# Performance work log

Hardware: AMD Instinct MI355X
Metric: run time of the kernel (lower is better)

Reference implementation:

```python
import jax, jax.numpy as jnp
import numpy as np

B, Q, C = 8, 100, 1024
H, W = 64, 64
NH = 16
HD = C // NH
SCALE = HD ** -0.5
LN_EPS = 1e-5


def setup_inputs() -> dict:
    key = jax.random.key(0)
    ks = jax.random.split(key, 8)
    xav = lambda k, shp: jax.random.normal(k, shp, jnp.float32) * (2.0 / (shp[0] + shp[-1])) ** 0.5
    return {
        "tgt": jax.random.normal(ks[0], (B, Q, C), jnp.float32),
        "memory": jax.random.normal(ks[1], (B, H, W, C), jnp.float32),
        "memory_pos_emb": jax.random.normal(ks[2], (B, H, W, C), jnp.float32),
        "query_pos_emb": jax.random.normal(ks[3], (B, Q, C), jnp.float32),
        "Wq": xav(ks[4], (C, C)),
        "Wk": xav(ks[5], (C, C)),
        "Wv": xav(ks[6], (C, C)),
        "Wo": xav(ks[7], (C, C)),
        "bo": jnp.zeros((C,), jnp.float32),
        "ln_gamma": jnp.ones((C,), jnp.float32),
        "ln_beta": jnp.zeros((C,), jnp.float32),
    }


def _layernorm(x, g, b):
    mu = jnp.mean(x, axis=-1, keepdims=True)
    var = jnp.var(x, axis=-1, keepdims=True)
    return (x - mu) * jax.lax.rsqrt(var + LN_EPS) * g + b


def reference(tgt, memory, memory_pos_emb, query_pos_emb, Wq, Wk, Wv, Wo, bo, ln_gamma, ln_beta):
    # flatten spatial dims: [B,H,W,C] -> [B,K,C]
    mem = memory.reshape(B, H * W, C)
    mpos = memory_pos_emb.reshape(B, H * W, C)
    q_in = tgt + query_pos_emb          # [B,Q,C]
    k_in = mem + mpos                    # [B,K,C]
    # projections (torch Linear: x @ W.T), split heads -> [B,nh,*,hd]
    q = (q_in @ Wq.T).reshape(B, Q, NH, HD).transpose(0, 2, 1, 3)
    k = (k_in @ Wk.T).reshape(B, -1, NH, HD).transpose(0, 2, 1, 3)
    v = (mem @ Wv.T).reshape(B, -1, NH, HD).transpose(0, 2, 1, 3)
    dots = jnp.einsum('bhid,bhjd->bhij', q, k) * SCALE   # [B,nh,Q,K]
    # slot attention: softmax over QUERY axis, then renormalize over keys
    attn = jax.nn.softmax(dots, axis=2)
    attn = attn / (jnp.sum(attn, axis=-1, keepdims=True) + 1e-8)
    updates = jnp.einsum('bhij,bhjd->bhid', attn, v)     # [B,nh,Q,hd]
    updates = updates.transpose(0, 2, 1, 3).reshape(B, Q, C)
    out = updates @ Wo.T + bo
    # residual (dropout is identity in eval) + post-LayerNorm
    return _layernorm(tgt + out, ln_gamma, ln_beta)
```

## Files before the change

kernel.cpp:

```cpp
#include <hip/hip_runtime.h>

typedef unsigned short u16;
typedef __attribute__((ext_vector_type(8))) short bf16x8;
typedef __attribute__((ext_vector_type(4))) short bf16x4;
typedef __attribute__((ext_vector_type(4))) float f32x4;
typedef __attribute__((ext_vector_type(4))) unsigned short u16x4;
typedef __attribute__((ext_vector_type(8))) unsigned short u16x8;
typedef __attribute__((ext_vector_type(4))) int i32x4;
typedef __attribute__((ext_vector_type(4))) float f4;

#define DI __device__ __forceinline__


DI u16 f2bf(float f){
  unsigned int u = __float_as_uint(f);
  return (u16)((u + 0x7FFFu + ((u >> 16) & 1u)) >> 16);
}

DI void gl_lds16(const void* g, void* l){
  __builtin_amdgcn_global_load_lds((const __attribute__((address_space(1))) unsigned int*)g,
                                   (__attribute__((address_space(3))) unsigned int*)l, 16, 0, 0);
}

__global__ __launch_bounds__(256) void prep_kv(const float* __restrict__ mem,
                                               const float* __restrict__ mpos,
                                               u16* __restrict__ kA, u16* __restrict__ vA){
  const int t = blockIdx.x * 256 + threadIdx.x;
  #pragma unroll
  for (int i = 0; i < 4; ++i){
    const size_t g = (size_t)t + (size_t)i * 1048576;
    f4 m0 = __builtin_nontemporal_load((const f4*)mem  + g * 2);
    f4 m1 = __builtin_nontemporal_load((const f4*)mem  + g * 2 + 1);
    f4 p0 = __builtin_nontemporal_load((const f4*)mpos + g * 2);
    f4 p1 = __builtin_nontemporal_load((const f4*)mpos + g * 2 + 1);
    u16x8 k, v;
    #pragma unroll
    for (int j = 0; j < 4; ++j){
      k[j]     = f2bf(m0[j] + p0[j]);  v[j]     = f2bf(m0[j]);
      k[j + 4] = f2bf(m1[j] + p1[j]);  v[j + 4] = f2bf(m1[j]);
    }
    ((u16x8*)kA)[g] = k;
    ((u16x8*)vA)[g] = v;
  }
}

__global__ __launch_bounds__(256) void prep_qw(const float* __restrict__ tgt,
                                               const float* __restrict__ qpos,
                                               const float* __restrict__ Wq, const float* __restrict__ Wk,
                                               const float* __restrict__ Wv, const float* __restrict__ Wo,
                                               u16* __restrict__ qA, u16* __restrict__ Wbf){
  int gid = blockIdx.x * 256 + threadIdx.x;
  const int NQ4 = 819200 / 4;
  if (gid < NQ4){
    f4 a = ((const f4*)tgt)[gid];
    f4 b = ((const f4*)qpos)[gid];
    u16x4 r;
    #pragma unroll
    for (int j = 0; j < 4; ++j) r[j] = f2bf(a[j] + b[j]);
    ((u16x4*)qA)[gid] = r;
  } else {
    int wid = gid - NQ4;
    int sel = wid >> 18;
    int off = wid & 262143;
    const float* W = (sel == 0) ? Wq : (sel == 1) ? Wk : (sel == 2) ? Wv : Wo;
    f4 w = ((const f4*)W)[off];
    u16x4 r;
    #pragma unroll
    for (int j = 0; j < 4; ++j) r[j] = f2bf(w[j]);
    ((u16x4*)(Wbf))[(size_t)sel * 262144 + off] = r;
  }
}

DI void gemm256_body(const u16* __restrict__ A, const u16* __restrict__ Bw,
                     u16* __restrict__ Cb, float scale, int sbid, int tid, char* lds)
{
  const int l = tid & 63, w = tid >> 6;
  const int mb = sbid >> 2, nb = sbid & 3;
  const int m0 = mb * 256, n0 = nb * 256;
  const int fr = l & 15, fg = l >> 4;
  const int wm = w >> 2, wn = w & 3;

  char* ldsA  = lds + wm * 8192 + l * 16;
  char* ldsB  = lds + 32768 + wn * 4096 + l * 16;
  char* ldsS0 = lds + w * 1024;
  char* ldsS1 = lds + (8 + w) * 1024;
  const u16* gA0 = A  + (size_t)(m0 + w * 16 + fr) * 1024 + fg * 8;
  const u16* gA1 = A  + (size_t)(m0 + (8 + w) * 16 + fr) * 1024 + fg * 8;
  const u16* gB0 = Bw + (size_t)(n0 + w * 16 + fr) * 1024 + fg * 8;
  const u16* gB1 = Bw + (size_t)(n0 + (8 + w) * 16 + fr) * 1024 + fg * 8;

  auto stA = [&](int pp, int kh, int kt){
    const int o = kt * 64 + kh * 32;
    gl_lds16(gA0 + o, ldsS0 + pp * 65536 + kh * 16384);
    gl_lds16(gA1 + o, ldsS1 + pp * 65536 + kh * 16384);
  };
  auto stB = [&](int pp, int kh, int kt){
    const int o = kt * 64 + kh * 32;
    gl_lds16(gB0 + o, ldsS0 + pp * 65536 + 32768 + kh * 16384);
    gl_lds16(gB1 + o, ldsS1 + pp * 65536 + 32768 + kh * 16384);
  };
  auto rdA4 = [&](bf16x8* av, int pp, int kh, int mfb){
    #pragma unroll
    for (int i = 0; i < 4; ++i)
      av[i] = *(const bf16x8*)(ldsA + pp * 65536 + kh * 16384 + (mfb + i) * 1024);
  };
  auto rdB4 = [&](bf16x8* bv, int pp, int kh){
    #pragma unroll
    for (int i = 0; i < 4; ++i)
      bv[i] = *(const bf16x8*)(ldsB + pp * 65536 + kh * 16384 + i * 1024);
  };

  f32x4 acc[8][4] = {};

  stA(0, 0, 0); stB(0, 0, 0); stA(0, 1, 0); stB(0, 1, 0);
  stA(1, 0, 1); stB(1, 0, 1);
  asm volatile("s_waitcnt vmcnt(8)" ::: "memory");
  __builtin_amdgcn_s_barrier();

  auto ktbody = [&](int P, int kt){
    const int kt1 = (kt + 1 > 15) ? 15 : kt + 1;
    const int kt2 = (kt + 2 > 15) ? 15 : kt + 2;
    bf16x8 av[4], bv[4];

    rdA4(av, P, 0, 0); rdB4(bv, P, 0);
    stA(P ^ 1, 1, kt1);
    __builtin_amdgcn_s_barrier();
    __builtin_amdgcn_s_setprio(1);
    #pragma unroll
    for (int i = 0; i < 4; ++i)
      #pragma unroll
      for (int n = 0; n < 4; ++n)
        acc[i][n] = __builtin_amdgcn_mfma_f32_16x16x32_bf16(av[i], bv[n], acc[i][n], 0, 0, 0);
    __builtin_amdgcn_s_setprio(0);
    __builtin_amdgcn_s_barrier();

    rdA4(av, P, 0, 4);
    stB(P ^ 1, 1, kt1);
    asm volatile("s_waitcnt vmcnt(8)" ::: "memory");
    __builtin_amdgcn_s_barrier();
    __builtin_amdgcn_s_setprio(1);
    #pragma unroll
    for (int i = 0; i < 4; ++i)
      #pragma unroll
      for (int n = 0; n < 4; ++n)
        acc[4 + i][n] = __builtin_amdgcn_mfma_f32_16x16x32_bf16(av[i], bv[n], acc[4 + i][n], 0, 0, 0);
    __builtin_amdgcn_s_setprio(0);
    __builtin_amdgcn_s_barrier();

    rdA4(av, P, 1, 0); rdB4(bv, P, 1);
    stA(P, 0, kt2);
    __builtin_amdgcn_s_barrier();
    __builtin_amdgcn_s_setprio(1);
    #pragma unroll
    for (int i = 0; i < 4; ++i)
      #pragma unroll
      for (int n = 0; n < 4; ++n)
        acc[i][n] = __builtin_amdgcn_mfma_f32_16x16x32_bf16(av[i], bv[n], acc[i][n], 0, 0, 0);
    __builtin_amdgcn_s_setprio(0);
    __builtin_amdgcn_s_barrier();

    rdA4(av, P, 1, 4);
    stB(P, 0, kt2);
    asm volatile("s_waitcnt vmcnt(8)" ::: "memory");
    __builtin_amdgcn_s_barrier();
    __builtin_amdgcn_s_setprio(1);
    #pragma unroll
    for (int i = 0; i < 4; ++i)
      #pragma unroll
      for (int n = 0; n < 4; ++n)
        acc[4 + i][n] = __builtin_amdgcn_mfma_f32_16x16x32_bf16(av[i], bv[n], acc[4 + i][n], 0, 0, 0);
    __builtin_amdgcn_s_setprio(0);
    __builtin_amdgcn_s_barrier();
  };

  for (int kk = 0; kk < 8; ++kk){
    ktbody(0, 2 * kk);
    ktbody(1, 2 * kk + 1);
  }

  asm volatile("s_waitcnt vmcnt(0)" ::: "memory");

  #pragma unroll
  for (int mf = 0; mf < 8; ++mf){
    #pragma unroll
    for (int nf = 0; nf < 4; ++nf){
      const int gcol = n0 + wn * 64 + nf * 16 + fr;
      #pragma unroll
      for (int r = 0; r < 4; ++r){
        const int grow = m0 + wm * 128 + mf * 16 + fg * 4 + r;
        Cb[(size_t)grow * 1024 + gcol] = f2bf(acc[mf][nf][r] * scale);
      }
    }
  }
}

__global__ __launch_bounds__(512, 1) void gemm256(
    const u16* __restrict__ A, const u16* __restrict__ Bw, u16* __restrict__ Cb)
{
  __shared__ __align__(16) char lds[131072];
  const int nwg = gridDim.x;
  const int sbid = (blockIdx.x & 7) * (nwg >> 3) + (blockIdx.x >> 3);
  gemm256_body(A, Bw, Cb, 1.0f, sbid, threadIdx.x, lds);
}

__global__ __launch_bounds__(512, 1) void gemm256kv(
    const u16* __restrict__ A0, const u16* __restrict__ B0, u16* __restrict__ C0,
    const u16* __restrict__ A1, const u16* __restrict__ B1, u16* __restrict__ C1)
{
  __shared__ __align__(16) char lds[131072];
  const int sel = blockIdx.x >> 9;
  const int inner = blockIdx.x & 511;
  const int sbid = (inner & 7) * 64 + (inner >> 3);
  if (sel == 0) gemm256_body(A0, B0, C0, 1.0f, sbid, threadIdx.x, lds);
  else          gemm256_body(A1, B1, C1, 1.0f, sbid, threadIdx.x, lds);
}

template<int MODE>
__global__ __launch_bounds__(256, 2) void gemm_bt(
    const u16* __restrict__ A, const u16* __restrict__ Bw,
    u16* __restrict__ Cb, float* __restrict__ Cf,
    const float* __restrict__ bias, const float* __restrict__ resid,
    int M, float scale)
{
  __shared__ u16 lA[2][128 * 32];
  __shared__ u16 lB[2][128 * 32];
  const int tid = threadIdx.x;
  const int l = tid & 63, w = tid >> 6;
  const int nwg = gridDim.x;
  int bid = blockIdx.x;
  bid = (bid & 7) * (nwg >> 3) + (bid >> 3);
  const int mb = bid >> 3, nb = bid & 7;
  const int m0 = mb * 128, n0 = nb * 128;
  const int fr = l & 15, fg = l >> 4;
  const int wr = w >> 1, wc = w & 1;

  f32x4 acc[4][4] = {};

  auto stage = [&](int buf, int kt){
    const int k0 = kt * 32;
    #pragma unroll
    for (int q = 0; q < 2; ++q){
      int r = w * 32 + q * 16 + (l >> 2);
      int ar = m0 + r; if (ar >= M) ar = M - 1;
      gl_lds16(A  + (size_t)ar * 1024 + k0 + (l & 3) * 8, &lA[buf][(w * 32 + q * 16) * 32]);
      gl_lds16(Bw + (size_t)(n0 + r) * 1024 + k0 + (l & 3) * 8, &lB[buf][(w * 32 + q * 16) * 32]);
    }
  };

  stage(0, 0);
  __syncthreads();
  for (int kt = 0; kt < 32; ++kt){
    const int cur = kt & 1;
    if (kt < 31) stage(cur ^ 1, kt + 1);
    bf16x8 av[4], bv[4];
    #pragma unroll
    for (int m = 0; m < 4; ++m)
      av[m] = *(const bf16x8*)&lA[cur][(wr * 64 + m * 16 + fr) * 32 + fg * 8];
    #pragma unroll
    for (int n = 0; n < 4; ++n)
      bv[n] = *(const bf16x8*)&lB[cur][(wc * 64 + n * 16 + fr) * 32 + fg * 8];
    #pragma unroll
    for (int m = 0; m < 4; ++m)
      #pragma unroll
      for (int n = 0; n < 4; ++n)
        acc[m][n] = __builtin_amdgcn_mfma_f32_16x16x32_bf16(av[m], bv[n], acc[m][n], 0, 0, 0);
    __syncthreads();
  }

  #pragma unroll
  for (int m = 0; m < 4; ++m){
    const int grow_base = m0 + wr * 64 + m * 16 + fg * 4;
    #pragma unroll
    for (int n = 0; n < 4; ++n){
      const int gcol = n0 + wc * 64 + n * 16 + fr;
      #pragma unroll
      for (int r = 0; r < 4; ++r){
        const int grow = grow_base + r;
        if (grow < M){
          const float v = acc[m][n][r];
          if (MODE == 0) Cb[(size_t)grow * 1024 + gcol] = f2bf(v * scale);
          else           Cf[(size_t)grow * 1024 + gcol] = v + bias[gcol] + resid[(size_t)grow * 1024 + gcol];
        }
      }
    }
  }
}

__global__ __launch_bounds__(64, 1) void attn_k(
    const u16* __restrict__ qp, const u16* __restrict__ kp, const u16* __restrict__ vp,
    float* __restrict__ updpart, float* __restrict__ rspart)
{
  const int bidx = blockIdx.x;
  const int c = bidx & 7, h = (bidx >> 3) & 15, b = bidx >> 7;
  const int bh = b * 16 + h;
  const int l = threadIdx.x;
  const int fr = l & 15, fg = l >> 4;

  __shared__ u16 qlds[112 * 64];
  __shared__ __align__(16) u16 vlds[2][16 * 64];

  for (int t = 0; t < 14; ++t){
    int chunk = t * 64 + l;
    int row = chunk >> 3, cb = chunk & 7;
    i32x4 val = {0, 0, 0, 0};
    if (row < 100)
      val = *(const i32x4*)(qp + (size_t)(b * 100 + row) * 1024 + h * 64 + cb * 8);
    *(i32x4*)((char*)qlds + row * 128 + ((cb ^ (row & 7)) * 16)) = val;
  }
  __syncthreads();

  bf16x8 qf[7][2];
  #pragma unroll
  for (int n = 0; n < 7; ++n)
    #pragma unroll
    for (int ks = 0; ks < 2; ++ks){
      int row = n * 16 + fr;
      int cb = ks * 4 + fg;
      qf[n][ks] = *(const bf16x8*)((const char*)qlds + row * 128 + ((cb ^ (row & 7)) * 16));
    }

  f32x4 acc[7][4] = {};
  float rs[7] = {};
  const f32x4 fz = {0.f, 0.f, 0.f, 0.f};
  const size_t kvbase = ((size_t)b * 4096) * 1024 + h * 64;
  const int j00 = c * 512;

  const u16* ksrc = kp + kvbase + (size_t)fr * 1024 + fg * 8;
  const u16* vsrc = vp + kvbase + (size_t)(l >> 3) * 1024 + (l & 7) * 8;

  auto loadK = [&](int t, bf16x8& k0, bf16x8& k1){
    const size_t ro = (size_t)(j00 + t * 16) * 1024;
    k0 = *(const bf16x8*)(ksrc + ro);
    k1 = *(const bf16x8*)(ksrc + ro + 32);
  };
  auto loadV = [&](int t, bf16x8& a, bf16x8& bb){
    const size_t ro = (size_t)(j00 + t * 16) * 1024;
    a  = *(const bf16x8*)(vsrc + ro);
    bb = *(const bf16x8*)(vsrc + ro + 8 * 1024);
  };
  auto writeV = [&](int buf, bf16x8 a, bf16x8 bb){
    *(bf16x8*)&vlds[buf][l * 8] = a;
    *(bf16x8*)&vlds[buf][512 + l * 8] = bb;
  };

  bf16x8 kc0, kc1, kn0, kn1, vn0, vn1;
  loadK(0, kc0, kc1);
  loadV(0, vn0, vn1);
  writeV(0, vn0, vn1);

  for (int t = 0; t < 32; ++t){
    const int cur = t & 1;
    if (t < 31){
      loadK(t + 1, kn0, kn1);
      loadV(t + 1, vn0, vn1);
    }

    f32x4 s[7];
    #pragma unroll
    for (int n = 0; n < 7; ++n){
      s[n] = __builtin_amdgcn_mfma_f32_16x16x32_bf16(kc0, qf[n][0], fz, 0, 0, 0);
      s[n] = __builtin_amdgcn_mfma_f32_16x16x32_bf16(kc1, qf[n][1], s[n], 0, 0, 0);
    }
    if (fr >= 4){ s[6][0] = -1e30f; s[6][1] = -1e30f; s[6][2] = -1e30f; s[6][3] = -1e30f; }

    float pv[7][4];
    #pragma unroll
    for (int r = 0; r < 4; ++r){
      float m = s[0][r];
      #pragma unroll
      for (int n = 1; n < 7; ++n) m = fmaxf(m, s[n][r]);
      m = fmaxf(m, __shfl_xor(m, 1)); m = fmaxf(m, __shfl_xor(m, 2));
      m = fmaxf(m, __shfl_xor(m, 4)); m = fmaxf(m, __shfl_xor(m, 8));
      float sum = 0.f;
      #pragma unroll
      for (int n = 0; n < 7; ++n){ float e = __expf(s[n][r] - m); pv[n][r] = e; sum += e; }
      sum += __shfl_xor(sum, 1); sum += __shfl_xor(sum, 2);
      sum += __shfl_xor(sum, 4); sum += __shfl_xor(sum, 8);
      float inv = 1.0f / sum;
      #pragma unroll
      for (int n = 0; n < 7; ++n) pv[n][r] *= inv;
    }

    bf16x4 pk[7];
    #pragma unroll
    for (int n = 0; n < 7; ++n){
      rs[n] += pv[n][0] + pv[n][1] + pv[n][2] + pv[n][3];
      bf16x4 t4;
      t4[0] = (short)f2bf(pv[n][0]); t4[1] = (short)f2bf(pv[n][1]);
      t4[2] = (short)f2bf(pv[n][2]); t4[3] = (short)f2bf(pv[n][3]);
      pk[n] = t4;
    }

    bf16x4 vf[4];
    #pragma unroll
    for (int dt = 0; dt < 4; ++dt){
      bf16x4 tv;
      #pragma unroll
      for (int jj = 0; jj < 4; ++jj)
        tv[jj] = (short)vlds[cur][(fg * 4 + jj) * 64 + dt * 16 + fr];
      vf[dt] = tv;
    }

    #pragma unroll
    for (int n = 0; n < 7; ++n)
      #pragma unroll
      for (int dt = 0; dt < 4; ++dt)
        acc[n][dt] = __builtin_amdgcn_mfma_f32_16x16x16bf16_1k(vf[dt], pk[n], acc[n][dt], 0, 0, 0);

    if (t < 31){
      writeV(cur ^ 1, vn0, vn1);
      kc0 = kn0; kc1 = kn1;
    }
  }

  #pragma unroll
  for (int n = 0; n < 7; ++n){
    float v = rs[n];
    v += __shfl_xor(v, 16); v += __shfl_xor(v, 32);
    if (l < 16) rspart[((size_t)c * 128 + bh) * 112 + n * 16 + l] = v;
  }
  float* ub = updpart + ((size_t)c * 128 + bh) * 64 * 112;
  #pragma unroll
  for (int n = 0; n < 7; ++n)
    #pragma unroll
    for (int dt = 0; dt < 4; ++dt)
      #pragma unroll
      for (int r = 0; r < 4; ++r){
        int d = dt * 16 + fg * 4 + r;
        int i = n * 16 + fr;
        ub[d * 112 + i] = acc[n][dt][r];
      }
}

__global__ __launch_bounds__(128) void nrm_k(const float* __restrict__ updpart,
                                             const float* __restrict__ rspart,
                                             u16* __restrict__ updn){
  const int bid = blockIdx.x;
  const int d = bid & 63, h = (bid >> 6) & 15, b = bid >> 10;
  const int bh = b * 16 + h;
  const int tid = threadIdx.x;
  const int i = (tid < 112) ? tid : 111;
  float sum = 0.f, rsum = 0.f;
  #pragma unroll
  for (int cc = 0; cc < 8; ++cc){
    sum  += updpart[(((size_t)cc * 128 + bh) * 64 + d) * 112 + i];
    rsum += rspart[((size_t)cc * 128 + bh) * 112 + i];
  }
  if (tid < 100)
    updn[((size_t)b * 100 + tid) * 1024 + h * 64 + d] = f2bf(sum / (rsum + 1e-8f));
}

__global__ __launch_bounds__(256) void ln_k(const float* __restrict__ x,
                                            const float* __restrict__ g,
                                            const float* __restrict__ be,
                                            float* __restrict__ out){
  const int row = blockIdx.x;
  const int tid = threadIdx.x;
  const f4 xv = *(const f4*)(x + (size_t)row * 1024 + tid * 4);
  float s = xv[0] + xv[1] + xv[2] + xv[3];
  float q = xv[0]*xv[0] + xv[1]*xv[1] + xv[2]*xv[2] + xv[3]*xv[3];
  #pragma unroll
  for (int m = 1; m < 64; m <<= 1){ s += __shfl_xor(s, m); q += __shfl_xor(q, m); }
  __shared__ float ss[4], qq[4];
  const int w = tid >> 6;
  if ((tid & 63) == 0){ ss[w] = s; qq[w] = q; }
  __syncthreads();
  s = ss[0] + ss[1] + ss[2] + ss[3];
  q = qq[0] + qq[1] + qq[2] + qq[3];
  const float mu = s * (1.0f / 1024.0f);
  const float var = q * (1.0f / 1024.0f) - mu * mu;
  const float rstd = rsqrtf(var + 1e-5f);
  const f4 gv = *(const f4*)(g + tid * 4);
  const f4 bv = *(const f4*)(be + tid * 4);
  f4 o;
  #pragma unroll
  for (int j = 0; j < 4; ++j) o[j] = (xv[j] - mu) * rstd * gv[j] + bv[j];
  *(f4*)(out + (size_t)row * 1024 + tid * 4) = o;
}

extern "C" void kernel_launch(void* const* d_in, const int* in_sizes, int n_in,
                              void* d_out, int out_size, void* d_ws, size_t ws_size,
                              hipStream_t stream)
{
  const float* tgt   = (const float*)d_in[0];
  const float* mem   = (const float*)d_in[1];
  const float* mpos  = (const float*)d_in[2];
  const float* qpos  = (const float*)d_in[3];
  const float* Wq    = (const float*)d_in[4];
  const float* Wk    = (const float*)d_in[5];
  const float* Wv    = (const float*)d_in[6];
  const float* Wo    = (const float*)d_in[7];
  const float* bo    = (const float*)d_in[8];
  const float* gamma = (const float*)d_in[9];
  const float* beta  = (const float*)d_in[10];

  char* ws = (char*)d_ws;
  u16* qA     = (u16*)(ws + 0);
  u16* Wbf    = (u16*)(ws + 1638400);
  u16* kA     = (u16*)(ws + 10027008);
  u16* vA     = (u16*)(ws + 77135872);
  u16* qproj  = (u16*)(ws + 144244736);
  u16* kproj  = (u16*)(ws + 145883136);
  float* updpart = (float*)(ws + 77135872);
  float* rspart  = (float*)(ws + 77135872 + 29360128);
  u16*   updn    = (u16*)  (ws + 77135872 + 29818880);
  float* resid   = (float*)(ws + 77135872 + 31457280);

  prep_kv<<<4096, 256, 0, stream>>>(mem, mpos, kA, vA);
  prep_qw<<<4896, 256, 0, stream>>>(tgt, qpos, Wq, Wk, Wv, Wo, qA, Wbf);
  gemm_bt<0><<<56, 256, 0, stream>>>(qA, Wbf, qproj, nullptr, nullptr, nullptr, 800, 0.125f);

  u16* vproj;
  if (ws_size >= (size_t)212992000 + 67108864){
    vproj = (u16*)(ws + 212992000);
    gemm256kv<<<1024, 512, 0, stream>>>(kA, Wbf + 1048576, kproj, vA, Wbf + 2097152, vproj);
  } else {
    vproj = kA;
    gemm256<<<512, 512, 0, stream>>>(kA, Wbf + 1048576, kproj);
    gemm256<<<512, 512, 0, stream>>>(vA, Wbf + 2097152, vproj);
  }

  attn_k<<<1024, 64, 0, stream>>>(qproj, kproj, vproj, updpart, rspart);
  nrm_k<<<8192, 128, 0, stream>>>(updpart, rspart, updn);
  gemm_bt<1><<<56, 256, 0, stream>>>(updn, Wbf + 3145728, nullptr, resid, bo, tgt, 800, 1.0f);
  ln_k<<<800, 256, 0, stream>>>(resid, gamma, beta, (float*)d_out);
}
```

Measured before the change: 383.6 us.

## Restructure 256x256 GEMM pipeline to one barrier phase per k-tile

```diff
diff --git a/kernel.cpp b/kernel.cpp
--- a/kernel.cpp
+++ b/kernel.cpp
@@ -99,10 +99,10 @@
     gl_lds16(gB0 + o, ldsS0 + pp * 65536 + 32768 + kh * 16384);
     gl_lds16(gB1 + o, ldsS1 + pp * 65536 + 32768 + kh * 16384);
   };
-  auto rdA4 = [&](bf16x8* av, int pp, int kh, int mfb){
-    #pragma unroll
-    for (int i = 0; i < 4; ++i)
-      av[i] = *(const bf16x8*)(ldsA + pp * 65536 + kh * 16384 + (mfb + i) * 1024);
+  auto rdA8 = [&](bf16x8* av, int pp, int kh){
+    #pragma unroll
+    for (int i = 0; i < 8; ++i)
+      av[i] = *(const bf16x8*)(ldsA + pp * 65536 + kh * 16384 + i * 1024);
   };
   auto rdB4 = [&](bf16x8* bv, int pp, int kh){
     #pragma unroll
@@ -112,64 +112,36 @@
 
   f32x4 acc[8][4] = {};
 
-  stA(0, 0, 0); stB(0, 0, 0); stA(0, 1, 0); stB(0, 1, 0);
-  stA(1, 0, 1); stB(1, 0, 1);
+  stA(0, 0, 0); stA(0, 1, 0); stB(0, 0, 0); stB(0, 1, 0);
+  stA(1, 0, 1); stA(1, 1, 1); stB(1, 0, 1); stB(1, 1, 1);
   asm volatile("s_waitcnt vmcnt(8)" ::: "memory");
   __builtin_amdgcn_s_barrier();
 
   auto ktbody = [&](int P, int kt){
-    const int kt1 = (kt + 1 > 15) ? 15 : kt + 1;
     const int kt2 = (kt + 2 > 15) ? 15 : kt + 2;
-    bf16x8 av[4], bv[4];
-
-    rdA4(av, P, 0, 0); rdB4(bv, P, 0);
-    stA(P ^ 1, 1, kt1);
+    bf16x8 a0[8], a1[8], b0[4], b1[4];
+
+    rdA8(a0, P, 0); rdA8(a1, P, 1);
+    rdB4(b0, P, 0); rdB4(b1, P, 1);
+    asm volatile("s_waitcnt lgkmcnt(0)" ::: "memory");
     __builtin_amdgcn_s_barrier();
+
+    stA(P, 0, kt2); stA(P, 1, kt2); stB(P, 0, kt2); stB(P, 1, kt2);
+
     __builtin_amdgcn_s_setprio(1);
     #pragma unroll
-    for (int i = 0; i < 4; ++i)
-      #pragma unroll
-      for (int n = 0; n < 4; ++n)
-        acc[i][n] = __builtin_amdgcn_mfma_f32_16x16x32_bf16(av[i], bv[n], acc[i][n], 0, 0, 0);
+    for (int mf = 0; mf < 8; ++mf)
+      #pragma unroll
+      for (int nf = 0; nf < 4; ++nf)
+        acc[mf][nf] = __builtin_amdgcn_mfma_f32_16x16x32_bf16(a0[mf], b0[nf], acc[mf][nf], 0, 0, 0);
+    #pragma unroll
+    for (int mf = 0; mf < 8; ++mf)
+      #pragma unroll
+      for (int nf = 0; nf < 4; ++nf)
+        acc[mf][nf] = __builtin_amdgcn_mfma_f32_16x16x32_bf16(a1[mf], b1[nf], acc[mf][nf], 0, 0, 0);
     __builtin_amdgcn_s_setprio(0);
-    __builtin_amdgcn_s_barrier();
-
-    rdA4(av, P, 0, 4);
-    stB(P ^ 1, 1, kt1);
+
     asm volatile("s_waitcnt vmcnt(8)" ::: "memory");
-    __builtin_amdgcn_s_barrier();
-    __builtin_amdgcn_s_setprio(1);
-    #pragma unroll
-    for (int i = 0; i < 4; ++i)
-      #pragma unroll
-      for (int n = 0; n < 4; ++n)
-        acc[4 + i][n] = __builtin_amdgcn_mfma_f32_16x16x32_bf16(av[i], bv[n], acc[4 + i][n], 0, 0, 0);
-    __builtin_amdgcn_s_setprio(0);
-    __builtin_amdgcn_s_barrier();
-
-    rdA4(av, P, 1, 0); rdB4(bv, P, 1);
-    stA(P, 0, kt2);
-    __builtin_amdgcn_s_barrier();
-    __builtin_amdgcn_s_setprio(1);
-    #pragma unroll
-    for (int i = 0; i < 4; ++i)
-      #pragma unroll
-      for (int n = 0; n < 4; ++n)
-        acc[i][n] = __builtin_amdgcn_mfma_f32_16x16x32_bf16(av[i], bv[n], acc[i][n], 0, 0, 0);
-    __builtin_amdgcn_s_setprio(0);
-    __builtin_amdgcn_s_barrier();
-
-    rdA4(av, P, 1, 4);
-    stB(P, 0, kt2);
-    asm volatile("s_waitcnt vmcnt(8)" ::: "memory");
-    __builtin_amdgcn_s_barrier();
-    __builtin_amdgcn_s_setprio(1);
-    #pragma unroll
-    for (int i = 0; i < 4; ++i)
-      #pragma unroll
-      for (int n = 0; n < 4; ++n)
-        acc[4 + i][n] = __builtin_amdgcn_mfma_f32_16x16x32_bf16(av[i], bv[n], acc[4 + i][n], 0, 0, 0);
-    __builtin_amdgcn_s_setprio(0);
     __builtin_amdgcn_s_barrier();
   };
 
@@ -194,7 +166,7 @@
   }
 }
 
-__global__ __launch_bounds__(512, 1) void gemm256(
+__global__ __launch_bounds__(512, 2) void gemm256(
     const u16* __restrict__ A, const u16* __restrict__ Bw, u16* __restrict__ Cb)
 {
   __shared__ __align__(16) char lds[131072];
@@ -203,7 +175,7 @@
   gemm256_body(A, Bw, Cb, 1.0f, sbid, threadIdx.x, lds);
 }
 
-__global__ __launch_bounds__(512, 1) void gemm256kv(
+__global__ __launch_bounds__(512, 2) void gemm256kv(
     const u16* __restrict__ A0, const u16* __restrict__ B0, u16* __restrict__ C0,
     const u16* __restrict__ A1, const u16* __restrict__ B1, u16* __restrict__ C1)
 {
```

Measured after the change: 397.9 us. 3.7% more time.
